# Kernel optimization log

Measured on AMD Instinct MI355X. Metric: run time of the kernel, lower is better.

Reference implementation:

```python
import jax, jax.numpy as jnp
import numpy as np

G = 32          # grid_size
H = 12          # num_heads
D = 768         # embed_dim
HD = D // H     # head_dim = 64
FF = 3072       # ff_dim
B, T = 2, 2048
SPAN = 2 * G - 1        # 63
SPAN_C = 4 * G + 1      # 129
EPS = 1e-5


def setup_inputs() -> dict:
    key = jax.random.key(0)
    ks = jax.random.split(key, 16)
    s = 0.02
    is_sep = jax.random.uniform(ks[6], (T,)) < 0.05
    demo_id = jax.random.randint(ks[5], (T,), 0, 8)
    demo_id = jnp.where(is_sep, -1, demo_id)
    return {
        'x': jax.random.normal(ks[0], (B, T, D), jnp.float32),
        'row': jax.random.randint(ks[1], (T,), 0, G),
        'col': jax.random.randint(ks[2], (T,), 0, G),
        'demo_row': jax.random.randint(ks[3], (T,), 0, G),
        'demo_col': jax.random.randint(ks[4], (T,), 0, 2 * G),
        'demo_id': demo_id,
        'is_sep': is_sep,
        'ln1_w': jnp.ones((D,), jnp.float32),
        'ln1_b': jnp.zeros((D,), jnp.float32),
        'ln2_w': jnp.ones((D,), jnp.float32),
        'ln2_b': jnp.zeros((D,), jnp.float32),
        'qkv_w': jax.random.normal(ks[7], (D, 3 * D), jnp.float32) * s,
        'qkv_b': jnp.zeros((3 * D,), jnp.float32),
        'proj_w': jax.random.normal(ks[8], (D, D), jnp.float32) * s,
        'proj_b': jnp.zeros((D,), jnp.float32),
        'ff1_w': jax.random.normal(ks[9], (D, FF), jnp.float32) * s,
        'ff1_b': jnp.zeros((FF,), jnp.float32),
        'ff2_w': jax.random.normal(ks[10], (FF, D), jnp.float32) * s,
        'ff2_b': jnp.zeros((D,), jnp.float32),
        'rel_emb': jax.random.normal(ks[11], (SPAN * SPAN, H), jnp.float32) * s,
        'demo_emb': jax.random.normal(ks[12], (SPAN_C * SPAN, H), jnp.float32) * s,
    }


def _ln(x, w, b):
    m = jnp.mean(x, -1, keepdims=True)
    v = jnp.mean((x - m) ** 2, -1, keepdims=True)
    return (x - m) / jnp.sqrt(v + EPS) * w + b


def _rel_bias(rel_emb, row, col, is_sep):
    g1 = G - 1
    dr = jnp.clip(row[:, None] - row[None, :], -g1, g1) + g1
    dc = jnp.clip(col[:, None] - col[None, :], -g1, g1) + g1
    bias = rel_emb[dr * SPAN + dc]              # (T, T, H)
    valid = ~is_sep
    vp = (valid[:, None] & valid[None, :]).astype(jnp.float32)
    return jnp.transpose(bias, (2, 0, 1)) * vp[None]  # (H, T, T)


def _demo_bias(demo_emb, drow, dcol, did, is_sep):
    g1 = G - 1
    dr = jnp.clip(drow[:, None] - drow[None, :], -g1, g1) + g1
    dc = jnp.clip(dcol[:, None] - dcol[None, :], -2 * G, 2 * G) + 2 * G
    bias = demo_emb[dr * SPAN_C + dc]           # (T, T, H)
    valid = ~is_sep
    same = (did[:, None] == did[None, :]) & (did[:, None] >= 0) & (did[None, :] >= 0)
    vp = (valid[:, None] & valid[None, :] & same).astype(jnp.float32)
    return jnp.transpose(bias, (2, 0, 1)) * vp[None]


def reference(x, row, col, demo_row, demo_col, demo_id, is_sep,
              ln1_w, ln1_b, ln2_w, ln2_b, qkv_w, qkv_b, proj_w, proj_b,
              ff1_w, ff1_b, ff2_w, ff2_b, rel_emb, demo_emb):
    b, t, d = x.shape
    h1 = _ln(x, ln1_w, ln1_b)
    qkv = h1 @ qkv_w + qkv_b                        # (B, T, 3D)
    q, k, v = jnp.split(qkv, 3, axis=-1)
    q = q.reshape(b, t, H, HD).transpose(0, 2, 1, 3)  # (B, H, T, HD)
    k = k.reshape(b, t, H, HD).transpose(0, 2, 1, 3)
    v = v.reshape(b, t, H, HD).transpose(0, 2, 1, 3)
    scale = float(HD) ** -0.5
    logits = jnp.einsum('bhqd,bhkd->bhqk', q, k) * scale
    bias = _rel_bias(rel_emb, row, col, is_sep) + _demo_bias(demo_emb, demo_row, demo_col, demo_id, is_sep)
    attn = jax.nn.softmax(logits + bias[None], axis=-1)
    out = jnp.einsum('bhqk,bhkd->bhqd', attn, v)
    out = out.transpose(0, 2, 1, 3).reshape(b, t, D)
    out = out @ proj_w + proj_b
    x = x + out
    h2 = _ln(x, ln2_w, ln2_b)
    ff = jax.nn.gelu(h2 @ ff1_w + ff1_b, approximate=False) @ ff2_w + ff2_b
    return x + ff
```

## Files before the change

kernel.cpp:

```cpp
#include <hip/hip_runtime.h>
#include <hip/hip_bf16.h>
#include <math.h>

#define G_ 32
#define H_ 12
#define D_ 768
#define HD_ 64
#define FF_ 3072
#define B_ 2
#define T_ 2048
#define SPAN_ 63
#define SPANC_ 129
#define EPSF 1e-5f

typedef short bf16x8 __attribute__((ext_vector_type(8)));
typedef short short4v __attribute__((ext_vector_type(4)));
typedef float f32x4 __attribute__((ext_vector_type(4)));

__device__ __forceinline__ short f2bf(float f) {
    unsigned u = __builtin_bit_cast(unsigned, f);
    u = u + 0x7FFFu + ((u >> 16) & 1u);
    return (short)(u >> 16);
}

__device__ __forceinline__ void gl_lds16(const void* g, void* l) {
    __builtin_amdgcn_global_load_lds(
        (const __attribute__((address_space(1))) unsigned int*)g,
        (__attribute__((address_space(3))) unsigned int*)l, 16, 0, 0);
}

__global__ __launch_bounds__(256) void ln_bf16_kernel(const float* __restrict__ x,
                                                      const float* __restrict__ w,
                                                      const float* __restrict__ b,
                                                      short* __restrict__ out) {
    int wv = threadIdx.x >> 6;
    int lane = threadIdx.x & 63;
    int rowi = blockIdx.x * 4 + wv;
    const float* xr = x + (size_t)rowi * D_;
    float vals[12];
    float s = 0.f;
#pragma unroll
    for (int i = 0; i < 12; ++i) { vals[i] = xr[lane + i * 64]; s += vals[i]; }
#pragma unroll
    for (int off = 32; off > 0; off >>= 1) s += __shfl_xor(s, off, 64);
    float mean = s * (1.0f / D_);
    float vs = 0.f;
#pragma unroll
    for (int i = 0; i < 12; ++i) { float d = vals[i] - mean; vs += d * d; }
#pragma unroll
    for (int off = 32; off > 0; off >>= 1) vs += __shfl_xor(vs, off, 64);
    float rstd = rsqrtf(vs * (1.0f / D_) + EPSF);
    short* outr = out + (size_t)rowi * D_;
#pragma unroll
    for (int i = 0; i < 12; ++i) {
        int c = lane + i * 64;
        outr[c] = f2bf((vals[i] - mean) * rstd * w[c] + b[c]);
    }
}

__global__ __launch_bounds__(256) void tcast_kernel(const float* __restrict__ W,
                                                    short* __restrict__ Wt,
                                                    int K, int N) {
    __shared__ float t[32][33];
    int n0 = blockIdx.x * 32, k0 = blockIdx.y * 32;
    int tid = threadIdx.x;
    int r = tid >> 3, c4 = (tid & 7) * 4;
    float4 v = *(const float4*)(W + (size_t)(k0 + r) * N + n0 + c4);
    t[r][c4 + 0] = v.x; t[r][c4 + 1] = v.y; t[r][c4 + 2] = v.z; t[r][c4 + 3] = v.w;
    __syncthreads();
    short4v o;
    o[0] = f2bf(t[c4 + 0][r]); o[1] = f2bf(t[c4 + 1][r]);
    o[2] = f2bf(t[c4 + 2][r]); o[3] = f2bf(t[c4 + 3][r]);
    *(short4v*)(Wt + (size_t)(n0 + r) * K + k0 + c4) = o;
}

__global__ __launch_bounds__(256) void bias_build(
    const int* __restrict__ rowp, const int* __restrict__ colp,
    const int* __restrict__ drowp, const int* __restrict__ dcolp,
    const int* __restrict__ didp,
    const float* __restrict__ rel_emb, const float* __restrict__ demo_emb,
    ushort* __restrict__ biasT) {
    __shared__ ushort patch[12][16][72];
    int k0 = blockIdx.x * 64, q0 = blockIdx.y * 16;
    int tid = threadIdx.x;
    int qi = tid >> 4, kq = (tid & 15) * 4;
    int q = q0 + qi;
    int idq = didp[q];
    int rq = rowp[q], cq = colp[q], drq = drowp[q], dcq = dcolp[q];
#pragma unroll
    for (int j = 0; j < 4; ++j) {
        int k = k0 + kq + j;
        int idk = didp[k];
        float4 v0 = {0.f, 0.f, 0.f, 0.f}, v1 = v0, v2 = v0;
        if (idq >= 0 && idk >= 0) {
            int dr = min(max(rq - rowp[k], -(G_ - 1)), G_ - 1) + (G_ - 1);
            int dc = min(max(cq - colp[k], -(G_ - 1)), G_ - 1) + (G_ - 1);
            const float* rp = rel_emb + (size_t)(dr * SPAN_ + dc) * 12;
            v0 = *(const float4*)rp;
            v1 = *(const float4*)(rp + 4);
            v2 = *(const float4*)(rp + 8);
            if (idq == idk) {
                int ddr = min(max(drq - drowp[k], -(G_ - 1)), G_ - 1) + (G_ - 1);
                int ddc = min(max(dcq - dcolp[k], -2 * G_), 2 * G_) + 2 * G_;
                const float* dp = demo_emb + (size_t)(ddr * SPANC_ + ddc) * 12;
                float4 w0 = *(const float4*)dp;
                float4 w1 = *(const float4*)(dp + 4);
                float4 w2 = *(const float4*)(dp + 8);
                v0.x += w0.x; v0.y += w0.y; v0.z += w0.z; v0.w += w0.w;
                v1.x += w1.x; v1.y += w1.y; v1.z += w1.z; v1.w += w1.w;
                v2.x += w2.x; v2.y += w2.y; v2.z += w2.z; v2.w += w2.w;
            }
        }
        float bv[12] = {v0.x, v0.y, v0.z, v0.w, v1.x, v1.y, v1.z, v1.w,
                        v2.x, v2.y, v2.z, v2.w};
        int kl = kq + j;
#pragma unroll
        for (int h = 0; h < 12; ++h) patch[h][qi][kl] = (ushort)f2bf(bv[h]);
    }
    __syncthreads();
    for (int c = tid; c < 1536; c += 256) {
        int rowid = c >> 3, off = (c & 7) * 8;
        int h = rowid >> 4, q2 = rowid & 15;
        *(bf16x8*)(biasT + (size_t)h * T_ * T_ + (size_t)(q0 + q2) * T_ + k0 + off) =
            *(const bf16x8*)&patch[h][q2][off];
    }
}

enum { EPI_NONE = 0, EPI_RES = 1, EPI_GELU = 2 };

template <int EPI, int BF16OUT>
__global__ __launch_bounds__(256, 2) void gemm_bf16(const short* __restrict__ A,
                                                    const short* __restrict__ Bt,
                                                    const float* __restrict__ bias,
                                                    const float* __restrict__ res,
                                                    void* __restrict__ Cv,
                                                    int M, int N, int K) {
    __shared__ short As[128 * 64];
    __shared__ short Bs[128 * 64];
    int tid = threadIdx.x;
    int l = tid & 63;
    int w = tid >> 6;
    int wm = w >> 1, wn = w & 1;
    int row0 = blockIdx.y * 128, col0 = blockIdx.x * 128;
    int g = l >> 4, c16 = l & 15;
    f32x4 zero = {0.f, 0.f, 0.f, 0.f};
    f32x4 acc[4][4];
#pragma unroll
    for (int m = 0; m < 4; ++m)
#pragma unroll
        for (int n = 0; n < 4; ++n) acc[m][n] = zero;

    int srow = w * 32 + (l >> 3);
    int sseg0 = (l & 7);

    for (int k0 = 0; k0 < K; k0 += 64) {
#pragma unroll
        for (int inst = 0; inst < 4; ++inst) {
            int arow = srow + inst * 8;
            int seg = sseg0 ^ (arow & 7);
            gl_lds16(A + (size_t)(row0 + arow) * K + k0 + seg * 8,
                     &As[(w * 32 + inst * 8) * 64]);
            gl_lds16(Bt + (size_t)(col0 + arow) * K + k0 + seg * 8,
                     &Bs[(w * 32 + inst * 8) * 64]);
        }
        __syncthreads();
#pragma unroll
        for (int dk = 0; dk < 2; ++dk) {
            bf16x8 af[4], bfr[4];
#pragma unroll
            for (int m = 0; m < 4; ++m) {
                int r = wm * 64 + m * 16 + c16;
                af[m] = *(const bf16x8*)&As[r * 64 + (((dk * 4 + g) ^ (r & 7)) << 3)];
            }
#pragma unroll
            for (int n = 0; n < 4; ++n) {
                int r = wn * 64 + n * 16 + c16;
                bfr[n] = *(const bf16x8*)&Bs[r * 64 + (((dk * 4 + g) ^ (r & 7)) << 3)];
            }
#pragma unroll
            for (int m = 0; m < 4; ++m)
#pragma unroll
                for (int n = 0; n < 4; ++n)
                    acc[m][n] = __builtin_amdgcn_mfma_f32_16x16x32_bf16(af[m], bfr[n], acc[m][n], 0, 0, 0);
        }
        __syncthreads();
    }

#pragma unroll
    for (int m = 0; m < 4; ++m)
#pragma unroll
        for (int n = 0; n < 4; ++n) {
            int rrow = row0 + wm * 64 + m * 16 + g * 4;
            int ccol = col0 + wn * 64 + n * 16 + c16;
            float bv = bias[ccol];
#pragma unroll
            for (int i = 0; i < 4; ++i) {
                float v = acc[m][n][i] + bv;
                if (EPI == EPI_GELU) v = 0.5f * v * (1.f + erff(v * 0.70710678118f));
                if (EPI == EPI_RES) v += res[(size_t)(rrow + i) * N + ccol];
                if (BF16OUT)
                    ((short*)Cv)[(size_t)(rrow + i) * N + ccol] = f2bf(v);
                else
                    ((float*)Cv)[(size_t)(rrow + i) * N + ccol] = v;
            }
        }
}

__global__ __launch_bounds__(256, 2) void attn_mfma(
    const short* __restrict__ qkv,
    const ushort* __restrict__ biasT,
    short* __restrict__ attn_o) {
    __shared__ short Ks[64 * 64];
    __shared__ short Vt[64 * 72];
    __shared__ short Pb[4][16 * 72];

    int tid = threadIdx.x, w = tid >> 6, l = tid & 63;
    int g = l >> 4, c16 = l & 15;
    int qt = blockIdx.x & 31, bh = blockIdx.x >> 5;
    int h = bh % H_, b = bh / H_;
    int q0 = qt * 64;
    const int QS = 3 * D_;
    const short* kvbase = qkv + (size_t)b * T_ * QS;

    bf16x8 qf[2];
    {
        int qrow = q0 + w * 16 + c16;
        const short* qp = kvbase + (size_t)qrow * QS + h * HD_;
#pragma unroll
        for (int dk = 0; dk < 2; ++dk) qf[dk] = *(const bf16x8*)(qp + dk * 32 + g * 8);
    }
    const ushort* bptr[4];
#pragma unroll
    for (int i = 0; i < 4; ++i)
        bptr[i] = biasT + (size_t)h * T_ * T_ + (size_t)(q0 + w * 16 + g * 4 + i) * T_;

    f32x4 zero = {0.f, 0.f, 0.f, 0.f};
    f32x4 oacc[4];
#pragma unroll
    for (int nf = 0; nf < 4; ++nf) oacc[nf] = zero;
    float lsum[4] = {0.f, 0.f, 0.f, 0.f};

    unsigned bvu[16];
#pragma unroll
    for (int nf = 0; nf < 4; ++nf)
#pragma unroll
        for (int i = 0; i < 4; ++i)
            bvu[nf * 4 + i] = bptr[i][nf * 16 + c16];

    for (int kb = 0; kb < T_; kb += 64) {
        unsigned bvn[16];
        {
            int kbn = (kb + 64) & (T_ - 1);
#pragma unroll
            for (int nf = 0; nf < 4; ++nf)
#pragma unroll
                for (int i = 0; i < 4; ++i)
                    bvn[nf * 4 + i] = bptr[i][kbn + nf * 16 + c16];
        }
#pragma unroll
        for (int p = 0; p < 2; ++p) {
            int sidx = p * 256 + tid;
            int row = sidx >> 3, cseg = sidx & 7;
            *(bf16x8*)&Ks[row * 64 + ((cseg ^ (row & 7)) << 3)] =
                *(const bf16x8*)(kvbase + (size_t)(kb + row) * QS + D_ + h * HD_ + cseg * 8);
        }
        {
            int vrow = tid >> 2, part = tid & 3;
            const short* vp = kvbase + (size_t)(kb + vrow) * QS + 2 * D_ + h * HD_ + part * 16;
            bf16x8 v0 = *(const bf16x8*)(vp);
            bf16x8 v1 = *(const bf16x8*)(vp + 8);
            int kchunk = vrow >> 3, kpos = vrow & 7;
#pragma unroll
            for (int j = 0; j < 8; ++j) {
                int d = part * 16 + j;
                Vt[d * 72 + (((kchunk ^ (d >> 3)) & 7) << 3) + kpos] = v0[j];
            }
#pragma unroll
            for (int j = 0; j < 8; ++j) {
                int d = part * 16 + 8 + j;
                Vt[d * 72 + (((kchunk ^ (d >> 3)) & 7) << 3) + kpos] = v1[j];
            }
        }
        __syncthreads();

        f32x4 sac[4];
#pragma unroll
        for (int nf = 0; nf < 4; ++nf) sac[nf] = zero;
#pragma unroll
        for (int dk = 0; dk < 2; ++dk) {
#pragma unroll
            for (int nf = 0; nf < 4; ++nf) {
                int r = nf * 16 + c16;
                bf16x8 kf = *(const bf16x8*)&Ks[r * 64 + (((dk * 4 + g) ^ (r & 7)) << 3)];
                sac[nf] = __builtin_amdgcn_mfma_f32_16x16x32_bf16(qf[dk], kf, sac[nf], 0, 0, 0);
            }
        }

        float pp[4][4];
#pragma unroll
        for (int nf = 0; nf < 4; ++nf)
#pragma unroll
            for (int i = 0; i < 4; ++i) {
                float bvf = __builtin_bit_cast(float, bvu[nf * 4 + i] << 16);
                float e = __expf(fmaf(sac[nf][i], 0.125f, bvf));
                pp[nf][i] = e;
                lsum[i] += e;
            }
        short* pbw = &Pb[w][0];
#pragma unroll
        for (int nf = 0; nf < 4; ++nf) {
            int chunkbase = nf * 2 + (c16 >> 3);
            int kpos = c16 & 7;
#pragma unroll
            for (int i = 0; i < 4; ++i)
                pbw[(g * 4 + i) * 72 + (((chunkbase ^ g) & 7) << 3) + kpos] = f2bf(pp[nf][i]);
        }
#pragma unroll
        for (int dk = 0; dk < 2; ++dk) {
            bf16x8 pa = *(const bf16x8*)&pbw[c16 * 72 + (((dk * 4 + g) ^ (c16 >> 2)) & 7) * 8];
#pragma unroll
            for (int nf = 0; nf < 4; ++nf) {
                int d = nf * 16 + c16;
                bf16x8 vb = *(const bf16x8*)&Vt[d * 72 + (((dk * 4 + g) ^ (d >> 3)) & 7) * 8];
                oacc[nf] = __builtin_amdgcn_mfma_f32_16x16x32_bf16(pa, vb, oacc[nf], 0, 0, 0);
            }
        }
#pragma unroll
        for (int j = 0; j < 16; ++j) bvu[j] = bvn[j];
        __syncthreads();
    }

#pragma unroll
    for (int i = 0; i < 4; ++i) {
#pragma unroll
        for (int off = 1; off < 16; off <<= 1) lsum[i] += __shfl_xor(lsum[i], off, 64);
    }

#pragma unroll
    for (int nf = 0; nf < 4; ++nf)
#pragma unroll
        for (int i = 0; i < 4; ++i) {
            float o = oacc[nf][i] / lsum[i];
            int qq = q0 + w * 16 + g * 4 + i;
            attn_o[(size_t)(b * T_ + qq) * D_ + h * HD_ + nf * 16 + c16] = f2bf(o);
        }
}

extern "C" void kernel_launch(void* const* d_in, const int* in_sizes, int n_in,
                              void* d_out, int out_size, void* d_ws, size_t ws_size,
                              hipStream_t stream) {
    const float* x = (const float*)d_in[0];
    const int* rowp = (const int*)d_in[1];
    const int* colp = (const int*)d_in[2];
    const int* drowp = (const int*)d_in[3];
    const int* dcolp = (const int*)d_in[4];
    const int* didp = (const int*)d_in[5];
    const float* ln1_w = (const float*)d_in[7];
    const float* ln1_b = (const float*)d_in[8];
    const float* ln2_w = (const float*)d_in[9];
    const float* ln2_b = (const float*)d_in[10];
    const float* qkv_w = (const float*)d_in[11];
    const float* qkv_b = (const float*)d_in[12];
    const float* proj_w = (const float*)d_in[13];
    const float* proj_b = (const float*)d_in[14];
    const float* ff1_w = (const float*)d_in[15];
    const float* ff1_b = (const float*)d_in[16];
    const float* ff2_w = (const float*)d_in[17];
    const float* ff2_b = (const float*)d_in[18];
    const float* rel_emb = (const float*)d_in[19];
    const float* demo_emb = (const float*)d_in[20];
    float* out = (float*)d_out;

    const int M = B_ * T_;
    char* p = (char*)d_ws;
    short* h1 = (short*)p;     p += (size_t)M * D_ * 2;
    short* qkvb = (short*)p;   p += (size_t)M * 3 * D_ * 2;
    short* attn_o = (short*)p; p += (size_t)M * D_ * 2;
    short* qkvt = (short*)p;   p += (size_t)(3 * D_) * D_ * 2;
    short* projt = (short*)p;  p += (size_t)D_ * D_ * 2;
    short* ff1t = (short*)p;   p += (size_t)FF_ * D_ * 2;
    short* ff2t = (short*)p;   p += (size_t)D_ * FF_ * 2;
    float* x2 = (float*)p;
    short* h2 = (short*)(p + (size_t)M * D_ * 4);
    short* ffact = (short*)(p + (size_t)M * D_ * 4 + (size_t)M * D_ * 2);
    ushort* biasT = (ushort*)p;

    bias_build<<<dim3(T_ / 64, T_ / 16), 256, 0, stream>>>(
        rowp, colp, drowp, dcolp, didp, rel_emb, demo_emb, biasT);
    tcast_kernel<<<dim3(3 * D_ / 32, D_ / 32), 256, 0, stream>>>(qkv_w, qkvt, D_, 3 * D_);
    tcast_kernel<<<dim3(D_ / 32, D_ / 32), 256, 0, stream>>>(proj_w, projt, D_, D_);
    tcast_kernel<<<dim3(FF_ / 32, D_ / 32), 256, 0, stream>>>(ff1_w, ff1t, D_, FF_);
    tcast_kernel<<<dim3(D_ / 32, FF_ / 32), 256, 0, stream>>>(ff2_w, ff2t, FF_, D_);

    ln_bf16_kernel<<<dim3(M / 4), 256, 0, stream>>>(x, ln1_w, ln1_b, h1);

    gemm_bf16<EPI_NONE, 1><<<dim3(3 * D_ / 128, M / 128), 256, 0, stream>>>(
        h1, qkvt, qkv_b, nullptr, qkvb, M, 3 * D_, D_);

    attn_mfma<<<dim3(B_ * H_ * (T_ / 64)), 256, 0, stream>>>(qkvb, biasT, attn_o);

    gemm_bf16<EPI_RES, 0><<<dim3(D_ / 128, M / 128), 256, 0, stream>>>(
        attn_o, projt, proj_b, x, x2, M, D_, D_);

    ln_bf16_kernel<<<dim3(M / 4), 256, 0, stream>>>(x2, ln2_w, ln2_b, h2);

    gemm_bf16<EPI_GELU, 1><<<dim3(FF_ / 128, M / 128), 256, 0, stream>>>(
        h2, ff1t, ff1_b, nullptr, ffact, M, FF_, D_);

    gemm_bf16<EPI_RES, 0><<<dim3(D_ / 128, M / 128), 256, 0, stream>>>(
        ffact, ff2t, ff2_b, x2, out, M, D_, FF_);
}
```

Before: 266.6 us.

## Double-buffer K/V tiles in LDS with register prefetch two tiles ahead

The attention kernel now keeps two LDS buffers for K and V. Global loads for tile t+2 are issued into registers while tile t is computed, and tile t+1 is written to the other buffer, so only one barrier per iteration is needed. The V transpose store is packed into 32-bit writes of two keys. Bias prefetch across iterations is dropped in favour of loading the bias inside each iteration. This raises LDS use, which may reduce occupancy, and the bias load latency is no longer hidden.

```diff
diff --git a/kernel.cpp b/kernel.cpp
--- a/kernel.cpp
+++ b/kernel.cpp
@@ -210,8 +210,8 @@
     const short* __restrict__ qkv,
     const ushort* __restrict__ biasT,
     short* __restrict__ attn_o) {
-    __shared__ short Ks[64 * 64];
-    __shared__ short Vt[64 * 72];
+    __shared__ short Ks[2][64 * 64];
+    __shared__ short Vt[2][64 * 72];
     __shared__ short Pb[4][16 * 72];
 
     int tid = threadIdx.x, w = tid >> 6, l = tid & 63;
@@ -226,63 +226,78 @@
     {
         int qrow = q0 + w * 16 + c16;
         const short* qp = kvbase + (size_t)qrow * QS + h * HD_;
-#pragma unroll
-        for (int dk = 0; dk < 2; ++dk) qf[dk] = *(const bf16x8*)(qp + dk * 32 + g * 8);
+        qf[0] = *(const bf16x8*)(qp + g * 8);
+        qf[1] = *(const bf16x8*)(qp + 32 + g * 8);
     }
     const ushort* bptr[4];
 #pragma unroll
     for (int i = 0; i < 4; ++i)
         bptr[i] = biasT + (size_t)h * T_ * T_ + (size_t)(q0 + w * 16 + g * 4 + i) * T_;
 
+    int krow = tid >> 3, kseg = tid & 7;
+    int kx = (kseg ^ (krow & 7)) << 3;
+    const short* kgp = kvbase + D_ + h * HD_ + kseg * 8;
+    int vk0 = (tid & 31) * 2, vd0 = (tid >> 5) * 8;
+    int vbase = ((((vk0 >> 3) ^ (vd0 >> 3)) & 7) << 3) + (vk0 & 7);
+    const short* vgp = kvbase + 2 * D_ + h * HD_ + vd0;
+
     f32x4 zero = {0.f, 0.f, 0.f, 0.f};
     f32x4 oacc[4];
 #pragma unroll
     for (int nf = 0; nf < 4; ++nf) oacc[nf] = zero;
     float lsum[4] = {0.f, 0.f, 0.f, 0.f};
 
-    unsigned bvu[16];
-#pragma unroll
-    for (int nf = 0; nf < 4; ++nf)
-#pragma unroll
-        for (int i = 0; i < 4; ++i)
-            bvu[nf * 4 + i] = bptr[i][nf * 16 + c16];
-
-    for (int kb = 0; kb < T_; kb += 64) {
-        unsigned bvn[16];
+    bf16x8 kr0, kr1, vr0, vr1;
+    kr0 = *(const bf16x8*)(kgp + (size_t)krow * QS);
+    kr1 = *(const bf16x8*)(kgp + (size_t)(krow + 32) * QS);
+    vr0 = *(const bf16x8*)(vgp + (size_t)vk0 * QS);
+    vr1 = *(const bf16x8*)(vgp + (size_t)(vk0 + 1) * QS);
+    *(bf16x8*)&Ks[0][krow * 64 + kx] = kr0;
+    *(bf16x8*)&Ks[0][(krow + 32) * 64 + kx] = kr1;
+#pragma unroll
+    for (int j = 0; j < 8; ++j) {
+        unsigned pr = (unsigned)(ushort)vr0[j] | ((unsigned)(ushort)vr1[j] << 16);
+        *(unsigned*)&Vt[0][(vd0 + j) * 72 + vbase] = pr;
+    }
+    {
+        const short* kg1 = kgp + (size_t)64 * QS;
+        const short* vg1 = vgp + (size_t)64 * QS;
+        kr0 = *(const bf16x8*)(kg1 + (size_t)krow * QS);
+        kr1 = *(const bf16x8*)(kg1 + (size_t)(krow + 32) * QS);
+        vr0 = *(const bf16x8*)(vg1 + (size_t)vk0 * QS);
+        vr1 = *(const bf16x8*)(vg1 + (size_t)(vk0 + 1) * QS);
+    }
+
+    for (int t = 0; t < 32; ++t) {
+        __syncthreads();
+        const short* KsC = Ks[t & 1];
+        const short* VtC = Vt[t & 1];
+        short* KsN = Ks[(t + 1) & 1];
+        short* VtN = Vt[(t + 1) & 1];
+        *(bf16x8*)&KsN[krow * 64 + kx] = kr0;
+        *(bf16x8*)&KsN[(krow + 32) * 64 + kx] = kr1;
+#pragma unroll
+        for (int j = 0; j < 8; ++j) {
+            unsigned pr = (unsigned)(ushort)vr0[j] | ((unsigned)(ushort)vr1[j] << 16);
+            *(unsigned*)&VtN[(vd0 + j) * 72 + vbase] = pr;
+        }
         {
-            int kbn = (kb + 64) & (T_ - 1);
-#pragma unroll
-            for (int nf = 0; nf < 4; ++nf)
-#pragma unroll
-                for (int i = 0; i < 4; ++i)
-                    bvn[nf * 4 + i] = bptr[i][kbn + nf * 16 + c16];
-        }
-#pragma unroll
-        for (int p = 0; p < 2; ++p) {
-            int sidx = p * 256 + tid;
-            int row = sidx >> 3, cseg = sidx & 7;
-            *(bf16x8*)&Ks[row * 64 + ((cseg ^ (row & 7)) << 3)] =
-                *(const bf16x8*)(kvbase + (size_t)(kb + row) * QS + D_ + h * HD_ + cseg * 8);
-        }
-        {
-            int vrow = tid >> 2, part = tid & 3;
-            const short* vp = kvbase + (size_t)(kb + vrow) * QS + 2 * D_ + h * HD_ + part * 16;
-            bf16x8 v0 = *(const bf16x8*)(vp);
-            bf16x8 v1 = *(const bf16x8*)(vp + 8);
-            int kchunk = vrow >> 3, kpos = vrow & 7;
-#pragma unroll
-            for (int j = 0; j < 8; ++j) {
-                int d = part * 16 + j;
-                Vt[d * 72 + (((kchunk ^ (d >> 3)) & 7) << 3) + kpos] = v0[j];
-            }
-#pragma unroll
-            for (int j = 0; j < 8; ++j) {
-                int d = part * 16 + 8 + j;
-                Vt[d * 72 + (((kchunk ^ (d >> 3)) & 7) << 3) + kpos] = v1[j];
-            }
-        }
-        __syncthreads();
-
+            int kb2 = ((t + 2) & 31) * 64;
+            const short* kg2 = kgp + (size_t)kb2 * QS;
+            const short* vg2 = vgp + (size_t)kb2 * QS;
+            kr0 = *(const bf16x8*)(kg2 + (size_t)krow * QS);
+            kr1 = *(const bf16x8*)(kg2 + (size_t)(krow + 32) * QS);
+            vr0 = *(const bf16x8*)(vg2 + (size_t)vk0 * QS);
+            vr1 = *(const bf16x8*)(vg2 + (size_t)(vk0 + 1) * QS);
+        }
+        int kb = t * 64;
+        float bv[16];
+#pragma unroll
+        for (int nf = 0; nf < 4; ++nf)
+#pragma unroll
+            for (int i = 0; i < 4; ++i)
+                bv[nf * 4 + i] =
+                    __builtin_bit_cast(float, (unsigned)bptr[i][kb + nf * 16 + c16] << 16);
         f32x4 sac[4];
 #pragma unroll
         for (int nf = 0; nf < 4; ++nf) sac[nf] = zero;
@@ -291,19 +306,16 @@
 #pragma unroll
             for (int nf = 0; nf < 4; ++nf) {
                 int r = nf * 16 + c16;
-                bf16x8 kf = *(const bf16x8*)&Ks[r * 64 + (((dk * 4 + g) ^ (r & 7)) << 3)];
+                bf16x8 kf = *(const bf16x8*)&KsC[r * 64 + (((dk * 4 + g) ^ (r & 7)) << 3)];
                 sac[nf] = __builtin_amdgcn_mfma_f32_16x16x32_bf16(qf[dk], kf, sac[nf], 0, 0, 0);
             }
         }
-
-        float pp[4][4];
 #pragma unroll
         for (int nf = 0; nf < 4; ++nf)
 #pragma unroll
             for (int i = 0; i < 4; ++i) {
-                float bvf = __builtin_bit_cast(float, bvu[nf * 4 + i] << 16);
-                float e = __expf(fmaf(sac[nf][i], 0.125f, bvf));
-                pp[nf][i] = e;
+                float e = __expf(fmaf(sac[nf][i], 0.125f, bv[nf * 4 + i]));
+                sac[nf][i] = e;
                 lsum[i] += e;
             }
         short* pbw = &Pb[w][0];
@@ -313,7 +325,7 @@
             int kpos = c16 & 7;
 #pragma unroll
             for (int i = 0; i < 4; ++i)
-                pbw[(g * 4 + i) * 72 + (((chunkbase ^ g) & 7) << 3) + kpos] = f2bf(pp[nf][i]);
+                pbw[(g * 4 + i) * 72 + (((chunkbase ^ g) & 7) << 3) + kpos] = f2bf(sac[nf][i]);
         }
 #pragma unroll
         for (int dk = 0; dk < 2; ++dk) {
@@ -321,13 +333,10 @@
 #pragma unroll
             for (int nf = 0; nf < 4; ++nf) {
                 int d = nf * 16 + c16;
-                bf16x8 vb = *(const bf16x8*)&Vt[d * 72 + (((dk * 4 + g) ^ (d >> 3)) & 7) * 8];
+                bf16x8 vb = *(const bf16x8*)&VtC[d * 72 + (((dk * 4 + g) ^ (d >> 3)) & 7) * 8];
                 oacc[nf] = __builtin_amdgcn_mfma_f32_16x16x32_bf16(pa, vb, oacc[nf], 0, 0, 0);
             }
         }
-#pragma unroll
-        for (int j = 0; j < 16; ++j) bvu[j] = bvn[j];
-        __syncthreads();
     }
 
 #pragma unroll
```

Result: no change. 262.9 us (-1.4%).
